# Kernel tuning notes

Hardware: AMD Instinct MI355X
Metric: run time of the kernel (lower is better)

## Reference

```python
import jax, jax.numpy as jnp
import numpy as np

HEAD_DIM = 64
N_HEADS = 32
N_KV = 8
ROPE_BASE = 500000.0
FREQ_CONFIG = {"factor": 32.0, "low_freq_factor": 1.0, "high_freq_factor": 4.0, "original_context_length": 8192}


def _rope_tables(head_dim, theta, n_pos, fc):
    # faithful to precompute_rope_params with llama3 freq scaling
    inv_freq = 1.0 / theta ** (np.arange(0, head_dim, 2, dtype=np.float32) / head_dim)
    low_wl = fc["original_context_length"] / fc["low_freq_factor"]
    high_wl = fc["original_context_length"] / fc["high_freq_factor"]
    wavelen = 2.0 * np.pi / inv_freq
    inv_l = np.where(wavelen > low_wl, inv_freq / fc["factor"], inv_freq)
    smooth = (fc["original_context_length"] / wavelen - fc["low_freq_factor"]) / (fc["high_freq_factor"] - fc["low_freq_factor"])
    smoothed = (1.0 - smooth) * (inv_freq / fc["factor"]) + smooth * inv_freq
    med = (wavelen <= low_wl) & (wavelen >= high_wl)
    inv_freq = np.where(med, smoothed, inv_l)
    pos = np.arange(n_pos, dtype=np.float32)
    angles = pos[:, None] * inv_freq[None, :]          # [T, head_dim/2]
    angles = np.concatenate([angles, angles], axis=1)  # [T, head_dim]
    return jnp.asarray(np.cos(angles), jnp.float32), jnp.asarray(np.sin(angles), jnp.float32)


def _apply_rope(x, cos, sin):
    # x: [b, h, t, d]; cos/sin: [t, d]
    d = x.shape[-1]
    x1, x2 = x[..., : d // 2], x[..., d // 2:]
    rotated = jnp.concatenate([-x2, x1], axis=-1)
    return x * cos[None, None] + rotated * sin[None, None]


def setup_inputs() -> dict:
    key = jax.random.key(0)
    ks = jax.random.split(key, 5)
    b, t, d = 1, 2048, 2048
    s = 0.02
    return {
        "x": jax.random.normal(ks[0], (b, t, d), jnp.float32),
        "Wq": jax.random.normal(ks[1], (d, d), jnp.float32) * s,
        "Wk": jax.random.normal(ks[2], (N_KV * HEAD_DIM, d), jnp.float32) * s,
        "Wv": jax.random.normal(ks[3], (N_KV * HEAD_DIM, d), jnp.float32) * s,
        "Wo": jax.random.normal(ks[4], (d, d), jnp.float32) * s,
        "start_pos": 0,
    }


def reference(x, Wq, Wk, Wv, Wo, start_pos):
    b, t, _ = x.shape
    cos, sin = _rope_tables(HEAD_DIM, ROPE_BASE, start_pos + t, FREQ_CONFIG)
    cos, sin = cos[start_pos:start_pos + t], sin[start_pos:start_pos + t]

    q = (x @ Wq.T).reshape(b, t, N_HEADS, HEAD_DIM).transpose(0, 2, 1, 3)  # [b,H,t,d]
    k = (x @ Wk.T).reshape(b, t, N_KV, HEAD_DIM).transpose(0, 2, 1, 3)     # [b,G,t,d]
    v = (x @ Wv.T).reshape(b, t, N_KV, HEAD_DIM).transpose(0, 2, 1, 3)

    q = _apply_rope(q, cos, sin)
    k = _apply_rope(k, cos, sin)

    n_rep = N_HEADS // N_KV
    k = jnp.repeat(k, n_rep, axis=1)  # [b,H,t,d]
    v = jnp.repeat(v, n_rep, axis=1)

    scores = jnp.einsum("bhqd,bhkd->bhqk", q, k)
    causal = jnp.triu(jnp.ones((t, t), bool), k=1)
    scores = jnp.where(causal[None, None], -jnp.inf, scores) / jnp.sqrt(jnp.float32(HEAD_DIM))
    weights = jax.nn.softmax(scores, axis=-1)
    ctx = jnp.einsum("bhqk,bhkd->bhqd", weights, v)
    ctx = ctx.transpose(0, 2, 1, 3).reshape(b, t, N_HEADS * HEAD_DIM)
    return ctx @ Wo.T
```

## Files before the change

### kernel.cpp

```cpp
#include <hip/hip_runtime.h>
#include <math.h>

#define T_SEQ 2048
#define D_MODEL 2048
#define HEAD_DIM 64
#define N_HEADS 32
#define N_KV 8

using short8 = __attribute__((ext_vector_type(8))) short;
using f32x4  = __attribute__((ext_vector_type(4))) float;
using f32x16 = __attribute__((ext_vector_type(16))) float;
using u32x4  = __attribute__((ext_vector_type(4))) unsigned int;

#define MFMA16(a, b, c) __builtin_amdgcn_mfma_f32_16x16x32_bf16(a, b, c, 0, 0, 0)
#define MFMA32(a, b, c) __builtin_amdgcn_mfma_f32_32x32x16_bf16(a, b, c, 0, 0, 0)

__device__ __forceinline__ unsigned short f2bf(float f) {
    unsigned int u = __builtin_bit_cast(unsigned int, f);
    u += 0x7fff + ((u >> 16) & 1);
    return (unsigned short)(u >> 16);
}
__device__ __forceinline__ void gld_lds16(const ushort* g, ushort* l) {
    __builtin_amdgcn_global_load_lds((const __attribute__((address_space(1))) void*)g,
                                     (__attribute__((address_space(3))) void*)l, 16, 0, 0);
}
__device__ __forceinline__ unsigned int cvtpk(float lo, float hi) {
    unsigned int r;
    asm("v_cvt_pk_bf16_f32 %0, %1, %2" : "=v"(r) : "v"(lo), "v"(hi));
    return r;
}
__device__ __forceinline__ void plswap(unsigned int& a, unsigned int& b) {
    auto r = __builtin_amdgcn_permlane32_swap(a, b, false, false);
    a = r[0];
    b = r[1];
}

__global__ __launch_bounds__(256) void rope_tables_kernel(float* __restrict__ cosT, float* __restrict__ sinT,
                                                          const int* __restrict__ start_pos, int T) {
    int idx = blockIdx.x * 256 + threadIdx.x;
    int t = idx >> 5;
    int i = idx & 31;
    float pos = (float)(start_pos[0] + t);
    float expo = (float)i / 32.0f;
    float inv_freq = 1.0f / powf(500000.0f, expo);
    const float two_pi = 6.283185307179586f;
    float wavelen = two_pi / inv_freq;
    const float low_wl = 8192.0f;
    const float high_wl = 2048.0f;
    float inv;
    if (wavelen > low_wl) {
        inv = inv_freq / 32.0f;
    } else if (wavelen < high_wl) {
        inv = inv_freq;
    } else {
        float smooth = (8192.0f / wavelen - 1.0f) / 3.0f;
        inv = (1.0f - smooth) * (inv_freq / 32.0f) + smooth * inv_freq;
    }
    float ang = pos * inv;
    cosT[i * T + t] = cosf(ang);
    sinT[i * T + t] = sinf(ang);
}

__global__ __launch_bounds__(256) void cast_all_kernel(
    const float* __restrict__ x, const float* __restrict__ wq,
    const float* __restrict__ wk, const float* __restrict__ wv,
    const float* __restrict__ wo,
    ushort* __restrict__ xb, ushort* __restrict__ wqb,
    ushort* __restrict__ wkb, ushort* __restrict__ wvb, ushort* __restrict__ wob) {
    int i = blockIdx.x * 256 + threadIdx.x;
    const float* src; ushort* dst; int off;
    if (i < 1048576)      { src = x;  dst = xb;  off = i; }
    else if (i < 2097152) { src = wq; dst = wqb; off = i - 1048576; }
    else if (i < 2359296) { src = wk; dst = wkb; off = i - 2097152; }
    else if (i < 2621440) { src = wv; dst = wvb; off = i - 2359296; }
    else                  { src = wo; dst = wob; off = i - 2621440; }
    float4 v = ((const float4*)src)[off];
    ushort4 o;
    o.x = f2bf(v.x); o.y = f2bf(v.y); o.z = f2bf(v.z); o.w = f2bf(v.w);
    ((ushort4*)dst)[off] = o;
}

__global__ __launch_bounds__(256) void gemm_qkv(
    const ushort* __restrict__ X, const ushort* __restrict__ Wqb,
    const ushort* __restrict__ Wkb, const ushort* __restrict__ Wvb,
    ushort* __restrict__ Qo, ushort* __restrict__ Ko, ushort* __restrict__ Vto,
    const float* __restrict__ cosT, const float* __restrict__ sinT,
    int T, int D) {
    __shared__ __align__(16) ushort As[2][2][2048];
    __shared__ __align__(16) ushort Bs[2][2][4096];
    const int tid = threadIdx.x;
    const int w = tid >> 6, l = tid & 63;
    const int m0 = blockIdx.x * 64;
    const int n0g = blockIdx.y * 128;

    const ushort* B;
    ushort* Cout;
    int n0, doRope;
    if (n0g < 2048)      { B = Wqb + (size_t)n0g * D;          Cout = Qo;  n0 = n0g;        doRope = 1; }
    else if (n0g < 2560) { B = Wkb + (size_t)(n0g - 2048) * D; Cout = Ko;  n0 = n0g - 2048; doRope = 1; }
    else                 { B = Wvb + (size_t)(n0g - 2560) * D; Cout = Vto; n0 = n0g - 2560; doRope = 0; }

    const int wm = (w >> 1) * 32, wn = (w & 1) * 64;
    const int lr = l & 15;
    const int quad = l >> 4;

    f32x4 zero = {0.f, 0.f, 0.f, 0.f};
    f32x4 acc[2][4];
#pragma unroll
    for (int i = 0; i < 2; ++i)
#pragma unroll
        for (int j = 0; j < 4; ++j) acc[i][j] = zero;

    const int srow = l >> 2;
    const int scg  = ((l & 3) ^ (srow & 3)) * 8;
    const ushort* Ag  = X + (size_t)(m0 + 16 * w + srow) * D + scg;
    const ushort* Bg0 = B + (size_t)(16 * (2 * w) + srow) * D + scg;
    const ushort* Bg1 = B + (size_t)(16 * (2 * w + 1) + srow) * D + scg;

#define GSTAGE(k0v, nb) { \
    gld_lds16(Ag  + (k0v),      &As[nb][0][w * 512]); \
    gld_lds16(Ag  + (k0v) + 32, &As[nb][1][w * 512]); \
    gld_lds16(Bg0 + (k0v),      &Bs[nb][0][(2 * w) * 512]); \
    gld_lds16(Bg0 + (k0v) + 32, &Bs[nb][1][(2 * w) * 512]); \
    gld_lds16(Bg1 + (k0v),      &Bs[nb][0][(2 * w + 1) * 512]); \
    gld_lds16(Bg1 + (k0v) + 32, &Bs[nb][1][(2 * w + 1) * 512]); }

    GSTAGE(0, 0);

    const int rsw = (quad ^ (lr & 3)) * 8;
    for (int k0 = 0; k0 < D; k0 += 64) {
        const int b = (k0 >> 6) & 1;
        __syncthreads();
        if (k0 + 64 < D) GSTAGE(k0 + 64, b ^ 1);
#pragma unroll
        for (int sub = 0; sub < 2; ++sub) {
            short8 af[2], bf[4];
#pragma unroll
            for (int i = 0; i < 2; ++i) af[i] = *(const short8*)&As[b][sub][(wm + i * 16 + lr) * 32 + rsw];
#pragma unroll
            for (int j = 0; j < 4; ++j) bf[j] = *(const short8*)&Bs[b][sub][(wn + j * 16 + lr) * 32 + rsw];
#pragma unroll
            for (int i = 0; i < 2; ++i)
#pragma unroll
                for (int j = 0; j < 4; ++j)
                    acc[i][j] = MFMA16(af[i], bf[j], acc[i][j]);
        }
    }
#undef GSTAGE

    const int mbase = m0 + wm + quad * 4;
    if (doRope) {
        const float qsc = (n0g < 2048) ? 0.18033688011112042f : 1.0f;
#pragma unroll
        for (int i = 0; i < 2; ++i) {
            int trow = mbase + i * 16;
#pragma unroll
            for (int j = 0; j < 2; ++j) {
                int i1 = lr + j * 16;
                float4 c4 = *(const float4*)&cosT[(size_t)i1 * T + trow];
                float4 s4 = *(const float4*)&sinT[(size_t)i1 * T + trow];
                int n1 = n0 + wn + lr + j * 16;
                int n2 = n1 + 32;
                size_t b1 = (size_t)(n1 >> 6) * ((size_t)T * 64) + (size_t)(n1 & 63);
                size_t b2 = (size_t)(n2 >> 6) * ((size_t)T * 64) + (size_t)(n2 & 63);
                float cs[4] = {c4.x, c4.y, c4.z, c4.w};
                float sn[4] = {s4.x, s4.y, s4.z, s4.w};
#pragma unroll
                for (int r = 0; r < 4; ++r) {
                    float x1 = acc[i][j][r], x2 = acc[i][j + 2][r];
                    Cout[b1 + (size_t)(trow + r) * 64] = f2bf((x1 * cs[r] - x2 * sn[r]) * qsc);
                    Cout[b2 + (size_t)(trow + r) * 64] = f2bf((x2 * cs[r] + x1 * sn[r]) * qsc);
                }
            }
        }
    } else {
#pragma unroll
        for (int i = 0; i < 2; ++i)
#pragma unroll
            for (int j = 0; j < 4; ++j) {
                int n = n0 + wn + lr + j * 16;
                int m = mbase + i * 16;
                ushort4 o;
                o.x = f2bf(acc[i][j][0]); o.y = f2bf(acc[i][j][1]);
                o.z = f2bf(acc[i][j][2]); o.w = f2bf(acc[i][j][3]);
                *(ushort4*)&Vto[(size_t)n * T + m] = o;
            }
    }
}

__global__ __launch_bounds__(256) void gemm_bt_f32(const ushort* __restrict__ A,
                                                   const ushort* __restrict__ B,
                                                   float* __restrict__ C,
                                                   int M, int N, int K) {
    __shared__ __align__(16) ushort As[2][2][2048];
    __shared__ __align__(16) ushort Bs[2][2][4096];
    const int tid = threadIdx.x;
    const int w = tid >> 6, l = tid & 63;
    const int m0 = blockIdx.x * 64, n0 = blockIdx.y * 128;
    const int wm = (w >> 1) * 32, wn = (w & 1) * 64;
    const int lr = l & 15;
    const int quad = l >> 4;

    f32x4 zero = {0.f, 0.f, 0.f, 0.f};
    f32x4 acc[2][4];
#pragma unroll
    for (int i = 0; i < 2; ++i)
#pragma unroll
        for (int j = 0; j < 4; ++j) acc[i][j] = zero;

    const int srow = l >> 2;
    const int scg  = ((l & 3) ^ (srow & 3)) * 8;
    const ushort* Ag  = A + (size_t)(m0 + 16 * w + srow) * K + scg;
    const ushort* Bg0 = B + (size_t)(n0 + 16 * (2 * w) + srow) * K + scg;
    const ushort* Bg1 = B + (size_t)(n0 + 16 * (2 * w + 1) + srow) * K + scg;

#define GSTAGE(k0v, nb) { \
    gld_lds16(Ag  + (k0v),      &As[nb][0][w * 512]); \
    gld_lds16(Ag  + (k0v) + 32, &As[nb][1][w * 512]); \
    gld_lds16(Bg0 + (k0v),      &Bs[nb][0][(2 * w) * 512]); \
    gld_lds16(Bg0 + (k0v) + 32, &Bs[nb][1][(2 * w) * 512]); \
    gld_lds16(Bg1 + (k0v),      &Bs[nb][0][(2 * w + 1) * 512]); \
    gld_lds16(Bg1 + (k0v) + 32, &Bs[nb][1][(2 * w + 1) * 512]); }

    GSTAGE(0, 0);

    const int rsw = (quad ^ (lr & 3)) * 8;
    for (int k0 = 0; k0 < K; k0 += 64) {
        const int b = (k0 >> 6) & 1;
        __syncthreads();
        if (k0 + 64 < K) GSTAGE(k0 + 64, b ^ 1);
#pragma unroll
        for (int sub = 0; sub < 2; ++sub) {
            short8 af[2], bf[4];
#pragma unroll
            for (int i = 0; i < 2; ++i) af[i] = *(const short8*)&As[b][sub][(wm + i * 16 + lr) * 32 + rsw];
#pragma unroll
            for (int j = 0; j < 4; ++j) bf[j] = *(const short8*)&Bs[b][sub][(wn + j * 16 + lr) * 32 + rsw];
#pragma unroll
            for (int i = 0; i < 2; ++i)
#pragma unroll
                for (int j = 0; j < 4; ++j)
                    acc[i][j] = MFMA16(af[i], bf[j], acc[i][j]);
        }
    }
#undef GSTAGE

    const int mbase = m0 + wm + quad * 4;
    const int nbase = n0 + wn + lr;
#pragma unroll
    for (int i = 0; i < 2; ++i)
#pragma unroll
        for (int j = 0; j < 4; ++j)
#pragma unroll
            for (int r = 0; r < 4; ++r)
                C[(size_t)(mbase + i * 16 + r) * N + (nbase + j * 16)] = acc[i][j][r];
}

__global__ __launch_bounds__(256, 2) void attn_mfma(const ushort* __restrict__ Q,
                                                    const ushort* __restrict__ K,
                                                    const ushort* __restrict__ Vt,
                                                    ushort* __restrict__ ctx, int T) {
    __shared__ __align__(16) ushort Ks[3][4096];
    __shared__ __align__(16) ushort Vs[3][4096];
    const int tid = threadIdx.x, w = tid >> 6, l = tid & 63;
    const int lq = l & 31, hi = l >> 5;
    const int hp = blockIdx.y;
    const int hk = hp >> 1;
    const int h  = 2 * hp + (w & 1);
    const int roff = (w >> 1) * 32;
    const int bx = blockIdx.x;
    const int qt = ((hp >> 3) & 1) ? (31 - bx) : bx;
    const int ntiles = qt + 1;
    const int qbase = qt * 64;
    const int qrow = qbase + roff + lq;
    const ushort* Kb = K + (size_t)hk * T * 64;
    const ushort* Vb = Vt + (size_t)hk * 64 * T;

    const int srow = l >> 3;
    const int sc   = ((l & 7) ^ srow) * 8;

    const ushort* Qrow = Q + ((size_t)h * T + qrow) * 64;
    short8 qf[4];
#pragma unroll
    for (int ks = 0; ks < 4; ++ks)
        qf[ks] = *(const short8*)(Qrow + ks * 16 + hi * 8);

    f32x16 oacc0, oacc1;
#pragma unroll
    for (int r = 0; r < 16; ++r) { oacc0[r] = 0.f; oacc1[r] = 0.f; }
    float ls[4] = {0.f, 0.f, 0.f, 0.f};

#define ASTAGE(kt, buf) do { \
    size_t _k0 = (size_t)(kt) * 64; \
    const int _c0 = 2 * w, _c1 = 2 * w + 1; \
    gld_lds16(Kb + (_k0 + _c0 * 8 + srow) * 64 + sc, &Ks[buf][_c0 * 512]); \
    gld_lds16(Kb + (_k0 + _c1 * 8 + srow) * 64 + sc, &Ks[buf][_c1 * 512]); \
    gld_lds16(Vb + (size_t)(_c0 * 8 + srow) * T + _k0 + sc, &Vs[buf][_c0 * 512]); \
    gld_lds16(Vb + (size_t)(_c1 * 8 + srow) * T + _k0 + sc, &Vs[buf][_c1 * 512]); \
} while (0)

    ASTAGE(0, 0);
    if (ntiles > 1) ASTAGE(1, 1);

    int b = 0;
    for (int kt = 0; kt < ntiles; ++kt) {
        if (kt + 1 < ntiles) asm volatile("s_waitcnt vmcnt(4)" ::: "memory");
        else                 asm volatile("s_waitcnt vmcnt(0)" ::: "memory");
        __builtin_amdgcn_s_barrier();
        __builtin_amdgcn_sched_barrier(0);
        if (kt + 2 < ntiles) {
            int bs = b + 2; if (bs >= 3) bs -= 3;
            ASTAGE(kt + 2, bs);
        }
        const int k0 = kt * 64;
        const bool last = (kt == ntiles - 1);
        const bool halfT = last && (roff == 0);

        f32x16 s0, s1;
#pragma unroll
        for (int r = 0; r < 16; ++r) { s0[r] = 0.f; s1[r] = 0.f; }
        __builtin_amdgcn_s_setprio(1);
#pragma unroll
        for (int ks = 0; ks < 4; ++ks) {
            const int c = ((ks * 2 + hi) ^ (lq & 7)) * 8;
            short8 kf0 = *(const short8*)&Ks[b][lq * 64 + c];
            s0 = MFMA32(kf0, qf[ks], s0);
        }
        if (!halfT) {
#pragma unroll
            for (int ks = 0; ks < 4; ++ks) {
                const int c = ((ks * 2 + hi) ^ (lq & 7)) * 8;
                short8 kf1 = *(const short8*)&Ks[b][(lq + 32) * 64 + c];
                s1 = MFMA32(kf1, qf[ks], s1);
            }
        }
        __builtin_amdgcn_s_setprio(0);

        f32x16 p0, p1;
        if (last) {
            if (roff == 0) {
#pragma unroll
                for (int r = 0; r < 16; ++r) {
                    const int kk = k0 + (r & 3) + 8 * (r >> 2) + 4 * hi;
                    p0[r] = (kk <= qrow) ? __builtin_amdgcn_exp2f(s0[r]) : 0.f;
                }
            } else {
#pragma unroll
                for (int r = 0; r < 16; ++r) p0[r] = __builtin_amdgcn_exp2f(s0[r]);
#pragma unroll
                for (int r = 0; r < 16; ++r) {
                    const int kk = k0 + 32 + (r & 3) + 8 * (r >> 2) + 4 * hi;
                    p1[r] = (kk <= qrow) ? __builtin_amdgcn_exp2f(s1[r]) : 0.f;
                }
            }
        } else {
#pragma unroll
            for (int r = 0; r < 16; ++r) p0[r] = __builtin_amdgcn_exp2f(s0[r]);
#pragma unroll
            for (int r = 0; r < 16; ++r) p1[r] = __builtin_amdgcn_exp2f(s1[r]);
        }
#pragma unroll
        for (int r = 0; r < 16; ++r) ls[r & 3] += p0[r];
        if (!halfT) {
#pragma unroll
            for (int r = 0; r < 16; ++r) ls[r & 3] += p1[r];
        }

        const int nks2 = halfT ? 2 : 4;
        __builtin_amdgcn_s_setprio(1);
        for (int ks2 = 0; ks2 < nks2; ++ks2) {
            const f32x16& pp = (ks2 < 2) ? p0 : p1;
            const int bse = (ks2 & 1) * 8;
            unsigned int a0 = cvtpk(pp[bse + 0], pp[bse + 1]);
            unsigned int a1 = cvtpk(pp[bse + 2], pp[bse + 3]);
            unsigned int b0 = cvtpk(pp[bse + 4], pp[bse + 5]);
            unsigned int b1 = cvtpk(pp[bse + 6], pp[bse + 7]);
            plswap(a0, b0);
            plswap(a1, b1);
            u32x4 tw = {a0, a1, b0, b1};
            short8 pf = __builtin_bit_cast(short8, tw);
            const int c = ((ks2 * 2 + hi) ^ (lq & 7)) * 8;
            short8 vf0 = *(const short8*)&Vs[b][lq * 64 + c];
            short8 vf1 = *(const short8*)&Vs[b][(lq + 32) * 64 + c];
            oacc0 = MFMA32(vf0, pf, oacc0);
            oacc1 = MFMA32(vf1, pf, oacc1);
        }
        __builtin_amdgcn_s_setprio(0);
        if (++b == 3) b = 0;
    }
#undef ASTAGE

    float vsum = (ls[0] + ls[1]) + (ls[2] + ls[3]);
    vsum += __shfl_xor(vsum, 32, 64);
    const float inv = 1.f / vsum;

    ushort* cp = ctx + (size_t)qrow * 2048 + h * 64;
#pragma unroll
    for (int g = 0; g < 4; ++g) {
        ushort4 o0, o1;
        o0.x = f2bf(oacc0[4 * g + 0] * inv); o0.y = f2bf(oacc0[4 * g + 1] * inv);
        o0.z = f2bf(oacc0[4 * g + 2] * inv); o0.w = f2bf(oacc0[4 * g + 3] * inv);
        *(ushort4*)&cp[g * 8 + hi * 4] = o0;
        o1.x = f2bf(oacc1[4 * g + 0] * inv); o1.y = f2bf(oacc1[4 * g + 1] * inv);
        o1.z = f2bf(oacc1[4 * g + 2] * inv); o1.w = f2bf(oacc1[4 * g + 3] * inv);
        *(ushort4*)&cp[32 + g * 8 + hi * 4] = o1;
    }
}

extern "C" void kernel_launch(void* const* d_in, const int* in_sizes, int n_in,
                              void* d_out, int out_size, void* d_ws, size_t ws_size,
                              hipStream_t stream) {
    const float* x  = (const float*)d_in[0];
    const float* Wq = (const float*)d_in[1];
    const float* Wk = (const float*)d_in[2];
    const float* Wv = (const float*)d_in[3];
    const float* Wo = (const float*)d_in[4];
    const int* start_pos = (const int*)d_in[5];
    float* out = (float*)d_out;

    const int T = T_SEQ, D = D_MODEL;
    const int KV = N_KV * HEAD_DIM;

    char* w = (char*)d_ws;
    float* cosT = (float*)w;            w += (size_t)32 * T * 4;
    float* sinT = (float*)w;            w += (size_t)32 * T * 4;
    ushort* xbf  = (ushort*)w;          w += (size_t)T * D * 2;
    ushort* wqbf = (ushort*)w;          w += (size_t)D * D * 2;
    ushort* wkbf = (ushort*)w;          w += (size_t)KV * D * 2;
    ushort* wvbf = (ushort*)w;          w += (size_t)KV * D * 2;
    ushort* wobf = (ushort*)w;          w += (size_t)D * D * 2;
    ushort* qbf  = (ushort*)w;          w += (size_t)N_HEADS * T * 64 * 2;
    ushort* kbf  = (ushort*)w;          w += (size_t)N_KV * T * 64 * 2;
    ushort* vtbf = (ushort*)w;          w += (size_t)N_KV * 64 * T * 2;
    ushort* ctxbf = xbf;

    rope_tables_kernel<<<dim3((T * 32) / 256), dim3(256), 0, stream>>>(cosT, sinT, start_pos, T);

    cast_all_kernel<<<dim3(14336), dim3(256), 0, stream>>>(x, Wq, Wk, Wv, Wo,
                                                           xbf, wqbf, wkbf, wvbf, wobf);

    gemm_qkv<<<dim3(T / 64, (D + 2 * KV) / 128), dim3(256), 0, stream>>>(
        xbf, wqbf, wkbf, wvbf, qbf, kbf, vtbf, cosT, sinT, T, D);

    attn_mfma<<<dim3(32, 16), dim3(256), 0, stream>>>(qbf, kbf, vtbf, ctxbf, T);

    gemm_bt_f32<<<dim3(T / 64, D / 128), dim3(256), 0, stream>>>(ctxbf, wobf, out, T, D, D);
}
```

Baseline: 210.4 us.

## Software-pipeline QK^T one tile ahead of softmax and PV in attention loop

Restructures the attention main loop so the QK^T MFMAs for the next K tile are issued before the exp/softmax and PV MFMAs of the current tile. A prologue computes the first tile's scores, and the vmcnt waits are tightened so both the current and next tiles are resident. The intent is to overlap the exp/VALU work with matrix-core work across tiles. In exchange it holds two extra 16-float score accumulators per lane, raising register pressure, and it waits for loads earlier.

```diff
diff --git a/kernel.cpp b/kernel.cpp
--- a/kernel.cpp
+++ b/kernel.cpp
@@ -299,42 +299,62 @@
     gld_lds16(Vb + (size_t)(_c1 * 8 + srow) * T + _k0 + sc, &Vs[buf][_c1 * 512]); \
 } while (0)
 
+#define QKT(bn, sd0, sd1, skip1) do { \
+    __builtin_amdgcn_s_setprio(1); \
+    _Pragma("unroll") \
+    for (int ks = 0; ks < 4; ++ks) { \
+        const int c = ((ks * 2 + hi) ^ (lq & 7)) * 8; \
+        short8 kf0 = *(const short8*)&Ks[bn][lq * 64 + c]; \
+        sd0 = MFMA32(kf0, qf[ks], sd0); \
+    } \
+    if (!(skip1)) { \
+        _Pragma("unroll") \
+        for (int ks = 0; ks < 4; ++ks) { \
+            const int c = ((ks * 2 + hi) ^ (lq & 7)) * 8; \
+            short8 kf1 = *(const short8*)&Ks[bn][(lq + 32) * 64 + c]; \
+            sd1 = MFMA32(kf1, qf[ks], sd1); \
+        } \
+    } \
+    __builtin_amdgcn_s_setprio(0); \
+} while (0)
+
     ASTAGE(0, 0);
-    if (ntiles > 1) ASTAGE(1, 1);
+    if (ntiles > 1) {
+        ASTAGE(1, 1);
+        asm volatile("s_waitcnt vmcnt(6)" ::: "memory");
+    } else {
+        asm volatile("s_waitcnt vmcnt(2)" ::: "memory");
+    }
+    __builtin_amdgcn_s_barrier();
+    __builtin_amdgcn_sched_barrier(0);
+
+    f32x16 s_cur0, s_cur1, s_next0, s_next1;
+#pragma unroll
+    for (int r = 0; r < 16; ++r) { s_cur0[r] = 0.f; s_cur1[r] = 0.f; }
+    QKT(0, s_cur0, s_cur1, (ntiles == 1) && (roff == 0));
 
     int b = 0;
     for (int kt = 0; kt < ntiles; ++kt) {
-        if (kt + 1 < ntiles) asm volatile("s_waitcnt vmcnt(4)" ::: "memory");
+        if (kt + 1 < ntiles) asm volatile("s_waitcnt vmcnt(2)" ::: "memory");
         else                 asm volatile("s_waitcnt vmcnt(0)" ::: "memory");
         __builtin_amdgcn_s_barrier();
         __builtin_amdgcn_sched_barrier(0);
+
+        const int k0 = kt * 64;
+        const bool last  = (kt == ntiles - 1);
+        const bool halfT = last && (roff == 0);
+
+        if (kt + 1 < ntiles) {
+            int bn = b + 1; if (bn == 3) bn = 0;
+            const bool halfN = (kt + 1 == ntiles - 1) && (roff == 0);
+#pragma unroll
+            for (int r = 0; r < 16; ++r) { s_next0[r] = 0.f; s_next1[r] = 0.f; }
+            QKT(bn, s_next0, s_next1, halfN);
+        }
         if (kt + 2 < ntiles) {
             int bs = b + 2; if (bs >= 3) bs -= 3;
             ASTAGE(kt + 2, bs);
         }
-        const int k0 = kt * 64;
-        const bool last = (kt == ntiles - 1);
-        const bool halfT = last && (roff == 0);
-
-        f32x16 s0, s1;
-#pragma unroll
-        for (int r = 0; r < 16; ++r) { s0[r] = 0.f; s1[r] = 0.f; }
-        __builtin_amdgcn_s_setprio(1);
-#pragma unroll
-        for (int ks = 0; ks < 4; ++ks) {
-            const int c = ((ks * 2 + hi) ^ (lq & 7)) * 8;
-            short8 kf0 = *(const short8*)&Ks[b][lq * 64 + c];
-            s0 = MFMA32(kf0, qf[ks], s0);
-        }
-        if (!halfT) {
-#pragma unroll
-            for (int ks = 0; ks < 4; ++ks) {
-                const int c = ((ks * 2 + hi) ^ (lq & 7)) * 8;
-                short8 kf1 = *(const short8*)&Ks[b][(lq + 32) * 64 + c];
-                s1 = MFMA32(kf1, qf[ks], s1);
-            }
-        }
-        __builtin_amdgcn_s_setprio(0);
 
         f32x16 p0, p1;
         if (last) {
@@ -342,22 +362,22 @@
 #pragma unroll
                 for (int r = 0; r < 16; ++r) {
                     const int kk = k0 + (r & 3) + 8 * (r >> 2) + 4 * hi;
-                    p0[r] = (kk <= qrow) ? __builtin_amdgcn_exp2f(s0[r]) : 0.f;
+                    p0[r] = (kk <= qrow) ? __builtin_amdgcn_exp2f(s_cur0[r]) : 0.f;
                 }
             } else {
 #pragma unroll
-                for (int r = 0; r < 16; ++r) p0[r] = __builtin_amdgcn_exp2f(s0[r]);
+                for (int r = 0; r < 16; ++r) p0[r] = __builtin_amdgcn_exp2f(s_cur0[r]);
 #pragma unroll
                 for (int r = 0; r < 16; ++r) {
                     const int kk = k0 + 32 + (r & 3) + 8 * (r >> 2) + 4 * hi;
-                    p1[r] = (kk <= qrow) ? __builtin_amdgcn_exp2f(s1[r]) : 0.f;
+                    p1[r] = (kk <= qrow) ? __builtin_amdgcn_exp2f(s_cur1[r]) : 0.f;
                 }
             }
         } else {
 #pragma unroll
-            for (int r = 0; r < 16; ++r) p0[r] = __builtin_amdgcn_exp2f(s0[r]);
-#pragma unroll
-            for (int r = 0; r < 16; ++r) p1[r] = __builtin_amdgcn_exp2f(s1[r]);
+            for (int r = 0; r < 16; ++r) p0[r] = __builtin_amdgcn_exp2f(s_cur0[r]);
+#pragma unroll
+            for (int r = 0; r < 16; ++r) p1[r] = __builtin_amdgcn_exp2f(s_cur1[r]);
         }
 #pragma unroll
         for (int r = 0; r < 16; ++r) ls[r & 3] += p0[r];
@@ -386,8 +406,12 @@
             oacc1 = MFMA32(vf1, pf, oacc1);
         }
         __builtin_amdgcn_s_setprio(0);
+
+        s_cur0 = s_next0;
+        s_cur1 = s_next1;
         if (++b == 3) b = 0;
     }
+#undef QKT
 #undef ASTAGE
 
     float vsum = (ls[0] + ls[1]) + (ls[2] + ls[3]);
```

Measured after the change: 206.1 us. -2.0%, faster.
